# Kernel optimization log

Measured on AMD Instinct MI355X. Metric: run time of the kernel, lower is better.

## Reference

```python
import jax, jax.numpy as jnp
import numpy as np

B_, S_, H_, I_, N_, K_ = 2, 2048, 1024, 2048, 16, 4

def setup_inputs() -> dict:
    key = jax.random.key(0)
    ks = jax.random.split(key, 6)
    return {
        "x": jax.random.normal(ks[0], (B_, S_, H_), jnp.float32),
        "W_in": jax.random.normal(ks[1], (H_, 2 * I_), jnp.float32) * (H_ ** -0.5),
        "conv_w": jax.random.normal(ks[2], (I_, 1, K_), jnp.float32) * (K_ ** -0.5),
        "ln_gamma": jnp.ones((I_,), jnp.float32),
        "ln_beta": jnp.zeros((I_,), jnp.float32),
        "W_xproj": jax.random.normal(ks[3], (I_, 2 * N_ + 1), jnp.float32) * (I_ ** -0.5),
        "A_param": jax.random.normal(ks[4], (I_, N_), jnp.float32) * 0.1,
        "D": jnp.ones((I_,), jnp.float32),
        "W_out": jax.random.normal(ks[5], (I_, H_), jnp.float32) * (I_ ** -0.5),
    }

def _layernorm(x, g, b, eps=1e-5):
    mu = jnp.mean(x, axis=-1, keepdims=True)
    var = jnp.mean((x - mu) ** 2, axis=-1, keepdims=True)
    return (x - mu) * jax.lax.rsqrt(var + eps) * g + b

def reference(x, W_in, conv_w, ln_gamma, ln_beta, W_xproj, A_param, D, W_out):
    b, s, _ = x.shape
    n = A_param.shape[1]
    xz = x @ W_in                                   # (b,s,2I)
    xc, z = jnp.split(xz, 2, axis=-1)
    # depthwise causal conv1d: torch pads both sides k-1 then truncates [:s] == left-pad k-1
    xc = jax.lax.conv_general_dilated(
        xc.transpose(0, 2, 1), conv_w, window_strides=(1,),
        padding=[(conv_w.shape[-1] - 1, 0)],
        feature_group_count=conv_w.shape[0],
        dimension_numbers=("NCH", "OIH", "NCH")).transpose(0, 2, 1)  # (b,s,I)
    xc = jax.nn.silu(xc)
    xc = _layernorm(xc, ln_gamma, ln_beta)
    xp = xc @ W_xproj                               # (b,s,2N+1)
    delta = jnp.clip(jax.nn.softplus(xp[..., :1]), 1e-6, 10.0)   # (b,s,1)
    Bm = xp[..., 1:1 + n]                           # (b,s,N)
    Cm = xp[..., 1 + n:]                            # (b,s,N)
    A = -jnp.clip(jax.nn.softplus(A_param), 0.1, 10.0)           # (I,N)
    # decay[b,s,i,n] = exp(delta[b,s] * A[i,n]), clamped
    decay = jnp.clip(jnp.exp(delta[..., None] * A[None, None]), 1e-6, 1.0)  # (b,s,I,N)
    # y = x * sum_n B*C*decay  (state-dim reduction of the broadcast 4D tensor)
    y = xc * jnp.einsum("bsn,bsin->bsi", Bm * Cm, decay)
    y = y + xc * D
    return (y * jax.nn.silu(z)) @ W_out
```

## Files before the change

### kernel.cpp

```cpp
#include <hip/hip_runtime.h>
#include <hip/hip_bf16.h>
#include <cmath>

typedef __bf16 bf16_t;
typedef __bf16 bf16x8 __attribute__((ext_vector_type(8)));
typedef __bf16 bf16x4 __attribute__((ext_vector_type(4)));
typedef float  f32x4  __attribute__((ext_vector_type(4)));

static constexpr int B_  = 2, S_ = 2048, H_ = 1024, I_ = 2048, NST = 16;
static constexpr int ROWS  = B_ * S_;
static constexpr int TWO_I = 2 * I_;
static constexpr int XPD   = 2 * NST + 1;
static constexpr int XPN   = 64;

#define AS_G(p) ((const __attribute__((address_space(1))) void*)(p))
#define AS_L(p) ((__attribute__((address_space(3))) void*)(p))

template<int N> __device__ __forceinline__ void wait_vmcnt();
template<> __device__ __forceinline__ void wait_vmcnt<4>() {
    asm volatile("s_waitcnt vmcnt(4)" ::: "memory");
}
template<> __device__ __forceinline__ void wait_vmcnt<8>() {
    asm volatile("s_waitcnt vmcnt(8)" ::: "memory");
}

__device__ __forceinline__ float softplus_f(float x) {
    return x > 15.f ? x : log1pf(__expf(x));
}

__device__ __forceinline__ f32x4 b2f(bf16x4 v) {
    return (f32x4){(float)v[0], (float)v[1], (float)v[2], (float)v[3]};
}

__device__ __forceinline__ float fast_exp2(float x) {
#if __has_builtin(__builtin_amdgcn_exp2f)
    return __builtin_amdgcn_exp2f(x);
#else
    return exp2f(x);
#endif
}
__device__ __forceinline__ float fast_rcp(float x) {
#if __has_builtin(__builtin_amdgcn_rcpf)
    return __builtin_amdgcn_rcpf(x);
#else
    return 1.f / x;
#endif
}
__device__ __forceinline__ float fast_sigmoid(float x) {
    return fast_rcp(1.f + __expf(-x));
}
__device__ __forceinline__ float rflf(float x) {
    return __int_as_float(__builtin_amdgcn_readfirstlane(__float_as_int(x)));
}

template<int GX, int GY, int XW>
__device__ __forceinline__ void xcd_swz(int id, int& bx, int& by) {
    constexpr int SX = GX / XW;
    constexpr int SY = GY * XW / 8;
    const int xcd = id & 7;
    const int j   = id >> 3;
    bx = (xcd % XW) * SX + j % SX;
    by = (xcd / XW) * SY + j / SX;
}


__global__ __launch_bounds__(256)
void prep_all(const float* __restrict__ x, const float* __restrict__ W_in,
              const float* __restrict__ W_out, const float* __restrict__ A_param,
              const float* __restrict__ Wx, const float* __restrict__ conv_w,
              bf16_t* __restrict__ Xb, bf16_t* __restrict__ W1t,
              bf16_t* __restrict__ Wot, float* __restrict__ A2T,
              float* __restrict__ cwT, bf16_t* __restrict__ WxTb)
{
    const int b   = blockIdx.x;
    const int tid = threadIdx.x;
    __shared__ float t[32][33];

    if (b < 4096) {
        const int i = b * 256 + tid;
        f32x4 v = *(const f32x4*)(x + (size_t)i * 4);
        bf16x4 o;
        o[0] = (bf16_t)v[0]; o[1] = (bf16_t)v[1];
        o[2] = (bf16_t)v[2]; o[3] = (bf16_t)v[3];
        *(bf16x4*)(Xb + (size_t)i * 4) = o;
    } else if (b < 8192) {
        const int tb = b - 4096;
        const int c0 = (tb & 127) * 32, r0 = (tb >> 7) * 32;
        const int tx = tid & 31, ty = tid >> 5;
        #pragma unroll
        for (int k = 0; k < 4; ++k)
            t[ty + 8 * k][tx] = W_in[(size_t)(r0 + ty + 8 * k) * 4096 + c0 + tx];
        __syncthreads();
        #pragma unroll
        for (int k = 0; k < 4; ++k)
            W1t[(size_t)(c0 + ty + 8 * k) * 1024 + r0 + tx] = (bf16_t)t[tx][ty + 8 * k];
    } else if (b < 10240) {
        const int tb = b - 8192;
        const int c0 = (tb & 31) * 32, r0 = (tb >> 5) * 32;
        const int tx = tid & 31, ty = tid >> 5;
        #pragma unroll
        for (int k = 0; k < 4; ++k)
            t[ty + 8 * k][tx] = W_out[(size_t)(r0 + ty + 8 * k) * 1024 + c0 + tx];
        __syncthreads();
        #pragma unroll
        for (int k = 0; k < 4; ++k)
            Wot[(size_t)(c0 + ty + 8 * k) * 2048 + r0 + tx] = (bf16_t)t[tx][ty + 8 * k];
    } else {
        const int i = (b - 10240) * 256 + tid;
        if (i < NST * I_) {
            int n = i >> 11, c = i & (I_ - 1);
            float sp = softplus_f(A_param[(size_t)c * NST + n]);
            A2T[i] = -fminf(fmaxf(sp, 0.1f), 10.f) * 1.44269504088896340736f;
        }
        if (i < 4 * I_) {
            int j = i >> 11, c = i & (I_ - 1);
            cwT[i] = conv_w[(size_t)c * 4 + j];
        }
        if (i < XPN * I_) {
            int j = i >> 11, c = i & (I_ - 1);
            WxTb[i] = (j < XPD) ? (bf16_t)Wx[(size_t)c * XPD + j] : (bf16_t)0.f;
        }
    }
}


template<int M, int N, int K, int GX, int GY, int XW>
__global__ __launch_bounds__(512)
void gemm1_8p(const bf16_t* __restrict__ A, const bf16_t* __restrict__ Bt,
              bf16_t* __restrict__ C)
{
    constexpr int BM = 256, BN = 256, BK = 64;
    constexpr int NKT = K / BK;
    constexpr int NIT = NKT / 2;

    __shared__ bf16_t lA[2 * 16384];
    __shared__ bf16_t lB[2 * 16384];

    int bx, by;
    xcd_swz<GX, GY, XW>(blockIdx.x, bx, by);
    const int bm = by * BM;
    const int bn = bx * BN;

    const int tid  = threadIdx.x;
    const int lane = tid & 63;
    const int wave = tid >> 6;
    const int wm   = wave >> 2;
    const int wn   = wave & 3;
    const int frow = lane & 15;
    const int ko   = lane >> 4;
    const int fr7  = frow & 7;

    const int str = tid >> 3;
    const int stp = tid & 7;

    const bf16_t* gA[4];
    const bf16_t* gB[4];
    #pragma unroll
    for (int h = 0; h < 2; ++h)
        #pragma unroll
        for (int a = 0; a < 2; ++a) {
            const int rt = h * 128 + a * 64 + str;
            gA[h * 2 + a] = A  + (size_t)(bm + rt) * K + ((stp ^ (str & 7)) << 3);
            gB[h * 2 + a] = Bt + (size_t)(bn + rt) * K + ((stp ^ (str & 7)) << 3);
        }
    const int ldst = wave * 512;

    f32x4 acc[8][4];
    #pragma unroll
    for (int m = 0; m < 8; ++m)
        #pragma unroll
        for (int n = 0; n < 4; ++n)
            acc[m][n] = (f32x4){0.f, 0.f, 0.f, 0.f};

    auto stageA2 = [&](int kt, int buf) {
        #pragma unroll
        for (int c = 0; c < 4; ++c)
            __builtin_amdgcn_global_load_lds(AS_G(gA[c] + kt * BK),
                AS_L(lA + buf * 16384 + c * 4096 + ldst), 16, 0, 0);
    };
    auto stageB2 = [&](int kt, int buf) {
        #pragma unroll
        for (int c = 0; c < 4; ++c)
            __builtin_amdgcn_global_load_lds(AS_G(gB[c] + kt * BK),
                AS_L(lB + buf * 16384 + c * 4096 + ldst), 16, 0, 0);
    };

    stageA2(0, 0); stageB2(0, 0);
    stageA2(1, 1); stageB2(1, 1);
    wait_vmcnt<8>();
    __builtin_amdgcn_s_barrier();

    #pragma unroll 1
    for (int it = 0; it < NIT; ++it) {
        #pragma unroll
        for (int half = 0; half < 2; ++half) {
            const int buf = half;
            const bf16_t* bufA = lA + buf * 16384;
            const bf16_t* bufB = lB + buf * 16384;
            int ktn = 2 * it + 2 + half;
            if (ktn >= NKT) ktn -= NKT;

            bf16x8 aF[8][2];
            bf16x8 bF[2][2];

            #pragma unroll
            for (int m = 0; m < 4; ++m)
                #pragma unroll
                for (int kh = 0; kh < 2; ++kh)
                    aF[m][kh] = *(const bf16x8*)(bufA + (wm * 128 + m * 16 + frow) * 64
                                                 + ((((kh << 2) | ko) ^ fr7) << 3));
            #pragma unroll
            for (int n = 0; n < 2; ++n)
                #pragma unroll
                for (int kh = 0; kh < 2; ++kh)
                    bF[n][kh] = *(const bf16x8*)(bufB + (wn * 64 + n * 16 + frow) * 64
                                                 + ((((kh << 2) | ko) ^ fr7) << 3));
            __builtin_amdgcn_s_barrier();
            asm volatile("s_waitcnt lgkmcnt(0)" ::: "memory");
            __builtin_amdgcn_sched_barrier(0);
            __builtin_amdgcn_s_setprio(1);
            #pragma unroll
            for (int m = 0; m < 4; ++m)
                #pragma unroll
                for (int n = 0; n < 2; ++n)
                    #pragma unroll
                    for (int kh = 0; kh < 2; ++kh)
                        acc[m][n] = __builtin_amdgcn_mfma_f32_16x16x32_bf16(
                            aF[m][kh], bF[n][kh], acc[m][n], 0, 0, 0);
            __builtin_amdgcn_s_setprio(0);
            __builtin_amdgcn_s_barrier();

            #pragma unroll
            for (int m = 0; m < 4; ++m)
                #pragma unroll
                for (int kh = 0; kh < 2; ++kh)
                    aF[4 + m][kh] = *(const bf16x8*)(bufA + (wm * 128 + (4 + m) * 16 + frow) * 64
                                                     + ((((kh << 2) | ko) ^ fr7) << 3));
            __builtin_amdgcn_s_barrier();
            asm volatile("s_waitcnt lgkmcnt(0)" ::: "memory");
            __builtin_amdgcn_sched_barrier(0);
            __builtin_amdgcn_s_setprio(1);
            #pragma unroll
            for (int m = 0; m < 4; ++m)
                #pragma unroll
                for (int n = 0; n < 2; ++n)
                    #pragma unroll
                    for (int kh = 0; kh < 2; ++kh)
                        acc[4 + m][n] = __builtin_amdgcn_mfma_f32_16x16x32_bf16(
                            aF[4 + m][kh], bF[n][kh], acc[4 + m][n], 0, 0, 0);
            __builtin_amdgcn_s_setprio(0);
            __builtin_amdgcn_s_barrier();

            #pragma unroll
            for (int n = 0; n < 2; ++n)
                #pragma unroll
                for (int kh = 0; kh < 2; ++kh)
                    bF[n][kh] = *(const bf16x8*)(bufB + (wn * 64 + (2 + n) * 16 + frow) * 64
                                                 + ((((kh << 2) | ko) ^ fr7) << 3));
            stageA2(ktn, buf);
            __builtin_amdgcn_s_barrier();
            asm volatile("s_waitcnt lgkmcnt(0)" ::: "memory");
            __builtin_amdgcn_sched_barrier(0);
            __builtin_amdgcn_s_setprio(1);
            #pragma unroll
            for (int m = 0; m < 4; ++m)
                #pragma unroll
                for (int n = 0; n < 2; ++n)
                    #pragma unroll
                    for (int kh = 0; kh < 2; ++kh)
                        acc[m][2 + n] = __builtin_amdgcn_mfma_f32_16x16x32_bf16(
                            aF[m][kh], bF[n][kh], acc[m][2 + n], 0, 0, 0);
            __builtin_amdgcn_s_setprio(0);
            __builtin_amdgcn_s_barrier();

            stageB2(ktn, buf);
            wait_vmcnt<8>();
            __builtin_amdgcn_s_barrier();
            __builtin_amdgcn_s_setprio(1);
            #pragma unroll
            for (int m = 0; m < 4; ++m)
                #pragma unroll
                for (int n = 0; n < 2; ++n)
                    #pragma unroll
                    for (int kh = 0; kh < 2; ++kh)
                        acc[4 + m][2 + n] = __builtin_amdgcn_mfma_f32_16x16x32_bf16(
                            aF[4 + m][kh], bF[n][kh], acc[4 + m][2 + n], 0, 0, 0);
            __builtin_amdgcn_s_setprio(0);
            __builtin_amdgcn_s_barrier();
        }
    }

    const int crow = (lane >> 4) * 4;
    const int ccol = lane & 15;
    #pragma unroll
    for (int m = 0; m < 8; ++m)
        #pragma unroll
        for (int n = 0; n < 4; ++n)
            #pragma unroll
            for (int r = 0; r < 4; ++r)
                C[(size_t)(bm + wm * 128 + m * 16 + crow + r) * N
                  + (bn + wn * 64 + n * 16 + ccol)] = (bf16_t)acc[m][n][r];
}


template<int M, int N, int K, int GX, int GY, int XW>
__global__ __launch_bounds__(512)
void gemm3_kg(const bf16_t* __restrict__ A, const bf16_t* __restrict__ Bt,
              float* __restrict__ C)
{
    constexpr int BM = 128, BN = 128, BK = 32;
    constexpr int KH = K / 2;
    constexpr int NT = KH / BK;
    constexpr int MR = 4, NR = 4, MH = 2;

    __shared__ bf16_t smem[65536];

    int bx, by;
    xcd_swz<GX, GY, XW>(blockIdx.x, bx, by);
    const int bm = by * BM;
    const int bn = bx * BN;

    const int tid  = threadIdx.x;
    const int lane = tid & 63;
    const int wave = tid >> 6;
    const int grp  = wave >> 2;
    const int gw   = wave & 3;
    const int wm   = gw >> 1;
    const int wn   = gw & 1;

    const int frow = lane & 15;
    const int fsw  = ((lane >> 4) ^ ((frow >> 1) & 3)) << 3;

    const int gtid = tid & 255;
    const int str  = gtid >> 2;
    const int stp  = gtid & 3;

    bf16_t* lA = smem + grp * 16384;
    bf16_t* lB = smem + 32768 + grp * 16384;

    const bf16_t* baseA[2];
    #pragma unroll
    for (int a = 0; a < 2; ++a) {
        const int rt = a * 64 + str;
        baseA[a] = A + (size_t)(bm + rt) * K + grp * KH + ((stp ^ ((rt >> 1) & 3)) << 3);
    }
    const bf16_t* baseB[2];
    #pragma unroll
    for (int a = 0; a < 2; ++a) {
        const int rt = a * 64 + str;
        baseB[a] = Bt + (size_t)(bn + rt) * K + grp * KH + ((stp ^ ((rt >> 1) & 3)) << 3);
    }

    f32x4 acc[MR][NR];
    #pragma unroll
    for (int m = 0; m < MR; ++m)
        #pragma unroll
        for (int n = 0; n < NR; ++n)
            acc[m][n] = (f32x4){0.f, 0.f, 0.f, 0.f};

    auto stageA = [&](int k0, int b) {
        #pragma unroll
        for (int a = 0; a < 2; ++a)
            __builtin_amdgcn_global_load_lds(AS_G(baseA[a] + k0),
                AS_L(lA + b * 4096 + a * 2048 + gw * 512), 16, 0, 0);
    };
    auto stageB = [&](int k0, int b) {
        #pragma unroll
        for (int a = 0; a < 2; ++a)
            __builtin_amdgcn_global_load_lds(AS_G(baseB[a] + k0),
                AS_L(lB + b * 4096 + a * 2048 + gw * 512), 16, 0, 0);
    };

    stageA(0, 0); stageB(0, 0);
    stageA(BK, 1); stageB(BK, 1);
    wait_vmcnt<4>();
    __builtin_amdgcn_s_barrier();

    #pragma unroll 1
    for (int t = 0; t < NT; ++t) {
        const int buf = t & 3;
        const int nb  = (t + 2) & 3;
        int kn = (t + 2) * BK;
        if (kn >= KH) kn -= KH;

        bf16x8 bfr[NR];
        #pragma unroll
        for (int n = 0; n < NR; ++n)
            bfr[n] = *(const bf16x8*)(lB + buf * 4096 + (wn * 64 + n * 16 + frow) * 32 + fsw);
        bf16x8 af0[MH];
        #pragma unroll
        for (int m = 0; m < MH; ++m)
            af0[m] = *(const bf16x8*)(lA + buf * 4096 + (wm * 64 + m * 16 + frow) * 32 + fsw);
        stageA(kn, nb);

        __builtin_amdgcn_s_setprio(1);
        #pragma unroll
        for (int m = 0; m < MH; ++m)
            #pragma unroll
            for (int n = 0; n < NR; ++n)
                acc[m][n] = __builtin_amdgcn_mfma_f32_16x16x32_bf16(
                    af0[m], bfr[n], acc[m][n], 0, 0, 0);
        __builtin_amdgcn_s_setprio(0);

        bf16x8 af1[MR - MH];
        #pragma unroll
        for (int m = 0; m < MR - MH; ++m)
            af1[m] = *(const bf16x8*)(lA + buf * 4096 + (wm * 64 + (MH + m) * 16 + frow) * 32 + fsw);
        stageB(kn, nb);

        __builtin_amdgcn_s_setprio(1);
        #pragma unroll
        for (int m = 0; m < MR - MH; ++m)
            #pragma unroll
            for (int n = 0; n < NR; ++n)
                acc[MH + m][n] = __builtin_amdgcn_mfma_f32_16x16x32_bf16(
                    af1[m], bfr[n], acc[MH + m][n], 0, 0, 0);
        __builtin_amdgcn_s_setprio(0);

        wait_vmcnt<4>();
        __builtin_amdgcn_s_barrier();
    }

    asm volatile("s_waitcnt vmcnt(0)" ::: "memory");
    __builtin_amdgcn_s_barrier();

    float* accx = (float*)smem;
    const int crow = (lane >> 4) * 4;
    const int ccol = lane & 15;

    if (grp == 1) {
        #pragma unroll
        for (int m = 0; m < MR; ++m)
            #pragma unroll
            for (int n = 0; n < NR; ++n) {
                const int row = wm * 64 + m * 16 + crow;
                const int col = wn * 64 + n * 16 + ccol;
                #pragma unroll
                for (int r = 0; r < 4; ++r)
                    accx[(size_t)(row + r) * 132 + col] = acc[m][n][r];
            }
    }
    __syncthreads();
    if (grp == 0) {
        #pragma unroll
        for (int m = 0; m < MR; ++m)
            #pragma unroll
            for (int n = 0; n < NR; ++n) {
                const int row = wm * 64 + m * 16 + crow;
                const int col = wn * 64 + n * 16 + ccol;
                #pragma unroll
                for (int r = 0; r < 4; ++r)
                    C[(size_t)(bm + row + r) * N + bn + col] =
                        acc[m][n][r] + accx[(size_t)(row + r) * 132 + col];
            }
    }
}


__global__ __launch_bounds__(256)
void conv_ln(const bf16_t* __restrict__ xz,
             const float* __restrict__ cwT,
             const float* __restrict__ ln_g,
             const float* __restrict__ ln_b,
             bf16_t* __restrict__ Xn)
{
    const int row  = blockIdx.x;
    const int s    = row & (S_ - 1);
    const int tid  = threadIdx.x;
    const int lane = tid & 63;
    const int wave = tid >> 6;
    const bf16_t* xzr = xz + (size_t)row * TWO_I;

    __shared__ float lnr[4][2];

    float xc[8];
    float sm = 0.f, sq = 0.f;

    #pragma unroll
    for (int g = 0; g < 2; ++g) {
        const int c = g * 1024 + tid * 4;
        const f32x4 w0 = *(const f32x4*)(cwT + 0 * I_ + c);
        const f32x4 w1 = *(const f32x4*)(cwT + 1 * I_ + c);
        const f32x4 w2 = *(const f32x4*)(cwT + 2 * I_ + c);
        const f32x4 w3 = *(const f32x4*)(cwT + 3 * I_ + c);
        const f32x4 z4 = (f32x4){0.f, 0.f, 0.f, 0.f};
        const f32x4 xv0 = (s >= 3) ? b2f(*(const bf16x4*)(xzr - 3 * TWO_I + c)) : z4;
        const f32x4 xv1 = (s >= 2) ? b2f(*(const bf16x4*)(xzr - 2 * TWO_I + c)) : z4;
        const f32x4 xv2 = (s >= 1) ? b2f(*(const bf16x4*)(xzr - 1 * TWO_I + c)) : z4;
        const f32x4 xv3 = b2f(*(const bf16x4*)(xzr + c));
        const f32x4 a = w0 * xv0 + w1 * xv1 + w2 * xv2 + w3 * xv3;
        #pragma unroll
        for (int e = 0; e < 4; ++e) {
            const float v = a[e];
            const float t = v * fast_sigmoid(v);
            xc[g * 4 + e] = t;
            sm += t; sq += t * t;
        }
    }

    #pragma unroll
    for (int off = 32; off; off >>= 1) {
        sm += __shfl_xor(sm, off, 64);
        sq += __shfl_xor(sq, off, 64);
    }
    if (lane == 0) { lnr[wave][0] = sm; lnr[wave][1] = sq; }
    __syncthreads();
    sm = lnr[0][0] + lnr[1][0] + lnr[2][0] + lnr[3][0];
    sq = lnr[0][1] + lnr[1][1] + lnr[2][1] + lnr[3][1];
    const float mu = sm * (1.f / I_);
    const float rs = rsqrtf(sq * (1.f / I_) - mu * mu + 1e-5f);

    #pragma unroll
    for (int g = 0; g < 2; ++g) {
        const int c = g * 1024 + tid * 4;
        const f32x4 gg = *(const f32x4*)(ln_g + c);
        const f32x4 bb = *(const f32x4*)(ln_b + c);
        bf16x4 h4;
        #pragma unroll
        for (int e = 0; e < 4; ++e)
            h4[e] = (bf16_t)((xc[g * 4 + e] - mu) * rs * gg[e] + bb[e]);
        *(bf16x4*)(Xn + (size_t)row * I_ + c) = h4;
    }
}


__global__ __launch_bounds__(256)
void xproj_gemm(const bf16_t* __restrict__ Xn,
                const bf16_t* __restrict__ Wb, float* __restrict__ xp_part)
{
    constexpr int BM = 128, BK = 32, KS = 512;
    __shared__ bf16_t lA[BM * BK];
    __shared__ bf16_t lB[XPN * BK];

    const int bm   = blockIdx.x * BM;
    const int ks   = blockIdx.y;
    const int tid  = threadIdx.x;
    const int lane = tid & 63;
    const int wave = tid >> 6;
    const int wm   = (wave >> 1) * 64;
    const int wn   = (wave & 1) * 32;

    const int srow  = lane >> 2;
    const int skoff = (lane & 3) * 8;
    const int frow  = lane & 15;
    const int fko   = (lane >> 4) * 8;

    f32x4 acc[4][2];
    #pragma unroll
    for (int m = 0; m < 4; ++m)
        #pragma unroll
        for (int n = 0; n < 2; ++n)
            acc[m][n] = (f32x4){0.f, 0.f, 0.f, 0.f};

    for (int k0 = ks * KS; k0 < ks * KS + KS; k0 += BK) {
        #pragma unroll
        for (int t = 0; t < 2; ++t) {
            const int c = wave * 2 + t;
            const bf16_t* ga = Xn + (size_t)(bm + c * 16 + srow) * I_ + k0 + skoff;
            __builtin_amdgcn_global_load_lds(AS_G(ga), AS_L(lA + c * 512), 16, 0, 0);
        }
        const bf16_t* gb = Wb + (size_t)(wave * 16 + srow) * I_ + k0 + skoff;
        __builtin_amdgcn_global_load_lds(AS_G(gb), AS_L(lB + wave * 512), 16, 0, 0);
        __syncthreads();

        bf16x8 af[4], bf2[2];
        #pragma unroll
        for (int m = 0; m < 4; ++m)
            af[m] = *(const bf16x8*)(lA + (wm + m * 16 + frow) * BK + fko);
        #pragma unroll
        for (int n = 0; n < 2; ++n)
            bf2[n] = *(const bf16x8*)(lB + (wn + n * 16 + frow) * BK + fko);

        #pragma unroll
        for (int m = 0; m < 4; ++m)
            #pragma unroll
            for (int n = 0; n < 2; ++n)
                acc[m][n] = __builtin_amdgcn_mfma_f32_16x16x32_bf16(
                    af[m], bf2[n], acc[m][n], 0, 0, 0);

        __syncthreads();
    }

    float* out = xp_part + ((size_t)ks * ROWS + bm) * XPN;
    const int crow = (lane >> 4) * 4;
    const int ccol = lane & 15;
    #pragma unroll
    for (int m = 0; m < 4; ++m)
        #pragma unroll
        for (int n = 0; n < 2; ++n)
            #pragma unroll
            for (int r = 0; r < 4; ++r)
                out[(size_t)(wm + m * 16 + crow + r) * XPN
                    + (wn + n * 16 + ccol)] = acc[m][n][r];
}


__global__ __launch_bounds__(256)
void ssm_gate(const bf16_t* __restrict__ xz,
              const bf16_t* __restrict__ Xn,
              const float* __restrict__ xp_part,
              const float* __restrict__ A2T,
              const float* __restrict__ Dv,
              bf16_t* __restrict__ U)
{
    const int row0 = blockIdx.x * 2;
    const int tid  = threadIdx.x;

    __shared__ float xps[2][XPD];
    __shared__ float bcs[2][NST];

    if (tid < XPD) {
        float s = 0.f;
        #pragma unroll
        for (int ks = 0; ks < 4; ++ks)
            s += xp_part[((size_t)ks * ROWS + row0) * XPN + tid];
        xps[0][tid] = s;
    } else if (tid >= 64 && tid < 64 + XPD) {
        const int j = tid - 64;
        float s = 0.f;
        #pragma unroll
        for (int ks = 0; ks < 4; ++ks)
            s += xp_part[((size_t)ks * ROWS + row0 + 1) * XPN + j];
        xps[1][j] = s;
    }
    __syncthreads();
    if (tid < NST)
        bcs[0][tid] = xps[0][1 + tid] * xps[0][1 + NST + tid];
    else if (tid >= 64 && tid < 64 + NST) {
        const int n = tid - 64;
        bcs[1][n] = xps[1][1 + n] * xps[1][1 + NST + n];
    }
    __syncthreads();

    const float d0 = fminf(fmaxf(softplus_f(xps[0][0]), 1e-6f), 10.f);
    const float d1 = fminf(fmaxf(softplus_f(xps[1][0]), 1e-6f), 10.f);

    const bf16_t* z0 = xz + (size_t)row0 * TWO_I + I_;
    const bf16_t* z1 = z0 + TWO_I;
    bf16_t* u0 = U + (size_t)row0 * I_;
    bf16_t* u1 = u0 + I_;

    #pragma unroll 1
    for (int g = 0; g < 2; ++g) {
        const int c = g * 1024 + tid * 4;
        f32x4 sa0 = (f32x4){0.f, 0.f, 0.f, 0.f};
        f32x4 sa1 = (f32x4){0.f, 0.f, 0.f, 0.f};
        #pragma unroll 1
        for (int nb = 0; nb < 4; ++nb) {
            const float* ap = A2T + (size_t)(nb * 4) * I_ + c;
            const f32x4 a0 = *(const f32x4*)(ap);
            const f32x4 a1 = *(const f32x4*)(ap + I_);
            const f32x4 a2 = *(const f32x4*)(ap + 2 * I_);
            const f32x4 a3 = *(const f32x4*)(ap + 3 * I_);
            const float b00 = rflf(bcs[0][nb * 4 + 0]), b10 = rflf(bcs[1][nb * 4 + 0]);
            const float b01 = rflf(bcs[0][nb * 4 + 1]), b11 = rflf(bcs[1][nb * 4 + 1]);
            const float b02 = rflf(bcs[0][nb * 4 + 2]), b12 = rflf(bcs[1][nb * 4 + 2]);
            const float b03 = rflf(bcs[0][nb * 4 + 3]), b13 = rflf(bcs[1][nb * 4 + 3]);
            #pragma unroll
            for (int e = 0; e < 4; ++e) {
                sa0[e] += b00 * fast_exp2(d0 * a0[e]);
                sa1[e] += b10 * fast_exp2(d1 * a0[e]);
                sa0[e] += b01 * fast_exp2(d0 * a1[e]);
                sa1[e] += b11 * fast_exp2(d1 * a1[e]);
                sa0[e] += b02 * fast_exp2(d0 * a2[e]);
                sa1[e] += b12 * fast_exp2(d1 * a2[e]);
                sa0[e] += b03 * fast_exp2(d0 * a3[e]);
                sa1[e] += b13 * fast_exp2(d1 * a3[e]);
            }
        }
        const f32x4 dvv = *(const f32x4*)(Dv + c);
        const f32x4 xn0 = b2f(*(const bf16x4*)(Xn + (size_t)row0 * I_ + c));
        const f32x4 xn1 = b2f(*(const bf16x4*)(Xn + (size_t)(row0 + 1) * I_ + c));
        const f32x4 zv0 = b2f(*(const bf16x4*)(z0 + c));
        const f32x4 zv1 = b2f(*(const bf16x4*)(z1 + c));
        bf16x4 o0, o1;
        #pragma unroll
        for (int e = 0; e < 4; ++e) {
            const float y0 = xn0[e] * (sa0[e] + dvv[e]);
            const float y1 = xn1[e] * (sa1[e] + dvv[e]);
            const float zz0 = zv0[e], zz1 = zv1[e];
            o0[e] = (bf16_t)(y0 * zz0 * fast_sigmoid(zz0));
            o1[e] = (bf16_t)(y1 * zz1 * fast_sigmoid(zz1));
        }
        *(bf16x4*)(u0 + c) = o0;
        *(bf16x4*)(u1 + c) = o1;
    }
}


extern "C" void kernel_launch(void* const* d_in, const int* in_sizes, int n_in,
                              void* d_out, int out_size, void* d_ws, size_t ws_size,
                              hipStream_t stream)
{
    const float* x     = (const float*)d_in[0];
    const float* W_in  = (const float*)d_in[1];
    const float* convw = (const float*)d_in[2];
    const float* ln_g  = (const float*)d_in[3];
    const float* ln_b  = (const float*)d_in[4];
    const float* Wx    = (const float*)d_in[5];
    const float* A_p   = (const float*)d_in[6];
    const float* Dv    = (const float*)d_in[7];
    const float* W_out = (const float*)d_in[8];
    float* out = (float*)d_out;

    char* ws = (char*)d_ws;
    bf16_t* Xb   = (bf16_t*)(ws);
    bf16_t* W1t  = (bf16_t*)(ws + (size_t)(8u  << 20));
    bf16_t* Wot  = (bf16_t*)(ws + (size_t)(16u << 20));
    float*  A2T  = (float*) (ws + (size_t)(20u << 20));
    float*  cwT  = (float*) (ws + (size_t)(20u << 20) + (128u << 10));
    bf16_t* WxTb = (bf16_t*)(ws + (size_t)(20u << 20) + (256u << 10));
    bf16_t* XZb  = (bf16_t*)(ws + (size_t)(22u << 20));
    bf16_t* U    = (bf16_t*)(ws + (size_t)(54u << 20));
    bf16_t* Xn   = (bf16_t*)(ws);
    float*  xp4  = (float*) (ws + (size_t)(86u << 20));

    prep_all<<<10752, 256, 0, stream>>>(x, W_in, W_out, A_p, Wx, convw,
                                        Xb, W1t, Wot, A2T, cwT, WxTb);

    gemm1_8p<ROWS, TWO_I, H_, 16, 16, 4>
        <<<256, 512, 0, stream>>>(Xb, W1t, XZb);
    conv_ln<<<ROWS, 256, 0, stream>>>(XZb, cwT, ln_g, ln_b, Xn);
    xproj_gemm<<<dim3(ROWS / 128, 4), 256, 0, stream>>>(Xn, WxTb, xp4);
    ssm_gate<<<ROWS / 2, 256, 0, stream>>>(XZb, Xn, xp4, A2T, Dv, U);
    gemm3_kg<ROWS, H_, I_, 8, 32, 2>
        <<<256, 512, 0, stream>>>(U, Wot, out);
}
```

Measured before the change: 127.3 us.

## Restructure gemm1 main loop with fewer barriers and reordered fragment reuse

The first GEMM's K-loop moves from an eight-phase schedule, with a barrier around every MFMA block, to a single loop over K tiles. All B fragments for the tile are loaded up front, and the two A halves are loaded in two steps. The MFMA blocks are reordered so each A half is reused across both B halves, which cuts the number of block barriers per tile from about eight to three. The explicit lgkmcnt waits and sched barriers before the compute blocks are removed, so the compiler now places the LDS waits; this risks different overlap or higher register pressure from holding more fragments at once.

```diff
diff --git a/kernel.cpp b/kernel.cpp
--- a/kernel.cpp
+++ b/kernel.cpp
@@ -126,12 +126,11 @@
 
 template<int M, int N, int K, int GX, int GY, int XW>
 __global__ __launch_bounds__(512)
-void gemm1_8p(const bf16_t* __restrict__ A, const bf16_t* __restrict__ Bt,
+void gemm1_bp(const bf16_t* __restrict__ A, const bf16_t* __restrict__ Bt,
               bf16_t* __restrict__ C)
 {
     constexpr int BM = 256, BN = 256, BK = 64;
     constexpr int NKT = K / BK;
-    constexpr int NIT = NKT / 2;
 
     __shared__ bf16_t lA[2 * 16384];
     __shared__ bf16_t lB[2 * 16384];
@@ -156,13 +155,11 @@
     const bf16_t* gA[4];
     const bf16_t* gB[4];
     #pragma unroll
-    for (int h = 0; h < 2; ++h)
-        #pragma unroll
-        for (int a = 0; a < 2; ++a) {
-            const int rt = h * 128 + a * 64 + str;
-            gA[h * 2 + a] = A  + (size_t)(bm + rt) * K + ((stp ^ (str & 7)) << 3);
-            gB[h * 2 + a] = Bt + (size_t)(bn + rt) * K + ((stp ^ (str & 7)) << 3);
-        }
+    for (int c = 0; c < 4; ++c) {
+        const int rt = c * 64 + str;
+        gA[c] = A  + (size_t)(bm + rt) * K + ((stp ^ (str & 7)) << 3);
+        gB[c] = Bt + (size_t)(bn + rt) * K + ((stp ^ (str & 7)) << 3);
+    }
     const int ldst = wave * 512;
 
     f32x4 acc[8][4];
@@ -185,109 +182,102 @@
                 AS_L(lB + buf * 16384 + c * 4096 + ldst), 16, 0, 0);
     };
 
+    auto rdA = [&](const bf16_t* bufA, int m, int kh) {
+        return *(const bf16x8*)(bufA + (wm * 128 + m * 16 + frow) * 64
+                                + ((((kh << 2) | ko) ^ fr7) << 3));
+    };
+    auto rdB = [&](const bf16_t* bufB, int n, int kh) {
+        return *(const bf16x8*)(bufB + (wn * 64 + n * 16 + frow) * 64
+                                + ((((kh << 2) | ko) ^ fr7) << 3));
+    };
+
     stageA2(0, 0); stageB2(0, 0);
     stageA2(1, 1); stageB2(1, 1);
     wait_vmcnt<8>();
     __builtin_amdgcn_s_barrier();
 
     #pragma unroll 1
-    for (int it = 0; it < NIT; ++it) {
-        #pragma unroll
-        for (int half = 0; half < 2; ++half) {
-            const int buf = half;
-            const bf16_t* bufA = lA + buf * 16384;
-            const bf16_t* bufB = lB + buf * 16384;
-            int ktn = 2 * it + 2 + half;
-            if (ktn >= NKT) ktn -= NKT;
-
-            bf16x8 aF[8][2];
-            bf16x8 bF[2][2];
-
-            #pragma unroll
-            for (int m = 0; m < 4; ++m)
-                #pragma unroll
-                for (int kh = 0; kh < 2; ++kh)
-                    aF[m][kh] = *(const bf16x8*)(bufA + (wm * 128 + m * 16 + frow) * 64
-                                                 + ((((kh << 2) | ko) ^ fr7) << 3));
+    for (int t = 0; t < NKT; ++t) {
+        const int buf = t & 1;
+        const bf16_t* bufA = lA + buf * 16384;
+        const bf16_t* bufB = lB + buf * 16384;
+        int ktn = t + 2;
+        if (ktn >= NKT) ktn -= NKT;
+
+        bf16x8 a0[8], a1[8], b0[4], b1[4];
+        #pragma unroll
+        for (int m = 0; m < 4; ++m)
+            #pragma unroll
+            for (int kh = 0; kh < 2; ++kh)
+                a0[m * 2 + kh] = rdA(bufA, m, kh);
+        #pragma unroll
+        for (int n = 0; n < 2; ++n)
+            #pragma unroll
+            for (int kh = 0; kh < 2; ++kh) {
+                b0[n * 2 + kh] = rdB(bufB, n, kh);
+                b1[n * 2 + kh] = rdB(bufB, 2 + n, kh);
+            }
+
+        __builtin_amdgcn_s_setprio(1);
+        #pragma unroll
+        for (int m = 0; m < 4; ++m)
             #pragma unroll
             for (int n = 0; n < 2; ++n)
                 #pragma unroll
                 for (int kh = 0; kh < 2; ++kh)
-                    bF[n][kh] = *(const bf16x8*)(bufB + (wn * 64 + n * 16 + frow) * 64
-                                                 + ((((kh << 2) | ko) ^ fr7) << 3));
-            __builtin_amdgcn_s_barrier();
-            asm volatile("s_waitcnt lgkmcnt(0)" ::: "memory");
-            __builtin_amdgcn_sched_barrier(0);
-            __builtin_amdgcn_s_setprio(1);
-            #pragma unroll
-            for (int m = 0; m < 4; ++m)
-                #pragma unroll
-                for (int n = 0; n < 2; ++n)
-                    #pragma unroll
-                    for (int kh = 0; kh < 2; ++kh)
-                        acc[m][n] = __builtin_amdgcn_mfma_f32_16x16x32_bf16(
-                            aF[m][kh], bF[n][kh], acc[m][n], 0, 0, 0);
-            __builtin_amdgcn_s_setprio(0);
-            __builtin_amdgcn_s_barrier();
-
-            #pragma unroll
-            for (int m = 0; m < 4; ++m)
-                #pragma unroll
-                for (int kh = 0; kh < 2; ++kh)
-                    aF[4 + m][kh] = *(const bf16x8*)(bufA + (wm * 128 + (4 + m) * 16 + frow) * 64
-                                                     + ((((kh << 2) | ko) ^ fr7) << 3));
-            __builtin_amdgcn_s_barrier();
-            asm volatile("s_waitcnt lgkmcnt(0)" ::: "memory");
-            __builtin_amdgcn_sched_barrier(0);
-            __builtin_amdgcn_s_setprio(1);
-            #pragma unroll
-            for (int m = 0; m < 4; ++m)
-                #pragma unroll
-                for (int n = 0; n < 2; ++n)
-                    #pragma unroll
-                    for (int kh = 0; kh < 2; ++kh)
-                        acc[4 + m][n] = __builtin_amdgcn_mfma_f32_16x16x32_bf16(
-                            aF[4 + m][kh], bF[n][kh], acc[4 + m][n], 0, 0, 0);
-            __builtin_amdgcn_s_setprio(0);
-            __builtin_amdgcn_s_barrier();
-
+                    acc[m][n] = __builtin_amdgcn_mfma_f32_16x16x32_bf16(
+                        a0[m * 2 + kh], b0[n * 2 + kh], acc[m][n], 0, 0, 0);
+        __builtin_amdgcn_s_setprio(0);
+
+        __builtin_amdgcn_s_setprio(1);
+        #pragma unroll
+        for (int m = 0; m < 4; ++m)
             #pragma unroll
             for (int n = 0; n < 2; ++n)
                 #pragma unroll
                 for (int kh = 0; kh < 2; ++kh)
-                    bF[n][kh] = *(const bf16x8*)(bufB + (wn * 64 + (2 + n) * 16 + frow) * 64
-                                                 + ((((kh << 2) | ko) ^ fr7) << 3));
-            stageA2(ktn, buf);
-            __builtin_amdgcn_s_barrier();
-            asm volatile("s_waitcnt lgkmcnt(0)" ::: "memory");
-            __builtin_amdgcn_sched_barrier(0);
-            __builtin_amdgcn_s_setprio(1);
-            #pragma unroll
-            for (int m = 0; m < 4; ++m)
+                    acc[m][2 + n] = __builtin_amdgcn_mfma_f32_16x16x32_bf16(
+                        a0[m * 2 + kh], b1[n * 2 + kh], acc[m][2 + n], 0, 0, 0);
+        __builtin_amdgcn_s_setprio(0);
+
+        #pragma unroll
+        for (int m = 0; m < 4; ++m)
+            #pragma unroll
+            for (int kh = 0; kh < 2; ++kh)
+                a1[m * 2 + kh] = rdA(bufA, 4 + m, kh);
+
+        __builtin_amdgcn_s_barrier();
+        __builtin_amdgcn_sched_barrier(0);
+        stageB2(ktn, buf);
+
+        __builtin_amdgcn_s_setprio(1);
+        #pragma unroll
+        for (int m = 0; m < 4; ++m)
+            #pragma unroll
+            for (int n = 0; n < 2; ++n)
                 #pragma unroll
-                for (int n = 0; n < 2; ++n)
-                    #pragma unroll
-                    for (int kh = 0; kh < 2; ++kh)
-                        acc[m][2 + n] = __builtin_amdgcn_mfma_f32_16x16x32_bf16(
-                            aF[m][kh], bF[n][kh], acc[m][2 + n], 0, 0, 0);
-            __builtin_amdgcn_s_setprio(0);
-            __builtin_amdgcn_s_barrier();
-
-            stageB2(ktn, buf);
-            wait_vmcnt<8>();
-            __builtin_amdgcn_s_barrier();
-            __builtin_amdgcn_s_setprio(1);
-            #pragma unroll
-            for (int m = 0; m < 4; ++m)
+                for (int kh = 0; kh < 2; ++kh)
+                    acc[4 + m][2 + n] = __builtin_amdgcn_mfma_f32_16x16x32_bf16(
+                        a1[m * 2 + kh], b1[n * 2 + kh], acc[4 + m][2 + n], 0, 0, 0);
+        __builtin_amdgcn_s_setprio(0);
+
+        __builtin_amdgcn_s_barrier();
+        __builtin_amdgcn_sched_barrier(0);
+        stageA2(ktn, buf);
+
+        __builtin_amdgcn_s_setprio(1);
+        #pragma unroll
+        for (int m = 0; m < 4; ++m)
+            #pragma unroll
+            for (int n = 0; n < 2; ++n)
                 #pragma unroll
-                for (int n = 0; n < 2; ++n)
-                    #pragma unroll
-                    for (int kh = 0; kh < 2; ++kh)
-                        acc[4 + m][2 + n] = __builtin_amdgcn_mfma_f32_16x16x32_bf16(
-                            aF[4 + m][kh], bF[n][kh], acc[4 + m][2 + n], 0, 0, 0);
-            __builtin_amdgcn_s_setprio(0);
-            __builtin_amdgcn_s_barrier();
-        }
+                for (int kh = 0; kh < 2; ++kh)
+                    acc[4 + m][n] = __builtin_amdgcn_mfma_f32_16x16x32_bf16(
+                        a1[m * 2 + kh], b0[n * 2 + kh], acc[4 + m][n], 0, 0, 0);
+        __builtin_amdgcn_s_setprio(0);
+
+        wait_vmcnt<8>();
+        __builtin_amdgcn_s_barrier();
     }
 
     const int crow = (lane >> 4) * 4;
@@ -718,7 +708,7 @@
     prep_all<<<10752, 256, 0, stream>>>(x, W_in, W_out, A_p, Wx, convw,
                                         Xb, W1t, Wot, A2T, cwT, WxTb);
 
-    gemm1_8p<ROWS, TWO_I, H_, 16, 16, 4>
+    gemm1_bp<ROWS, TWO_I, H_, 16, 16, 4>
         <<<256, 512, 0, stream>>>(Xb, W1t, XZb);
     conv_ln<<<ROWS, 256, 0, stream>>>(XZb, cwT, ln_g, ln_b, Xn);
     xproj_gemm<<<dim3(ROWS / 128, 4), 256, 0, stream>>>(Xn, WxTb, xp4);
```

Result: no change. 125.0 us (-1.8%).
